# Kernel tuning notes

Hardware: AMD Instinct MI355X
Metric: run time of the kernel (lower is better)

The kernel has to match this reference:

```python
import jax, jax.numpy as jnp
import numpy as np

ORDER = 2
TEMP = 1.0
NEG = -9e15


def setup_inputs() -> dict:
    key = jax.random.key(0)
    ks = jax.random.split(key, 12)
    B, D, N, L = 8, 64, 1024, 12
    C_OUT, NH, S = 64, 2, 2
    NOUT = (NH + 1) * ORDER * S + 1  # 13
    sc = 0.05
    x = jax.random.normal(ks[0], (B, D, N, L), jnp.float32)
    A = jax.random.uniform(ks[1], (S, N, N), jnp.float32)
    support = jnp.where(A > 0.9, A, 0.0)
    nv1 = jax.random.normal(ks[2], (N, D), jnp.float32)
    nv2 = jax.random.normal(ks[3], (D, N), jnp.float32)
    key_w = jax.random.normal(ks[4], (NH, 2 * C_OUT, D, L), jnp.float32) * sc
    key_b = jax.random.normal(ks[5], (NH, 2 * C_OUT), jnp.float32) * sc
    query_w = jax.random.normal(ks[6], (NH, 2 * C_OUT, D, L), jnp.float32) * sc
    query_b = jax.random.normal(ks[7], (NH, 2 * C_OUT), jnp.float32) * sc
    attn_w = jax.random.normal(ks[8], (NOUT, D * NOUT), jnp.float32) * sc
    attn_b = jax.random.normal(ks[9], (NOUT,), jnp.float32) * sc
    final_w = jax.random.normal(ks[10], (C_OUT, D), jnp.float32) * sc
    final_b = jax.random.normal(ks[11], (C_OUT,), jnp.float32) * sc
    return {"x": x, "support": support, "nv1": nv1, "nv2": nv2,
            "key_w": key_w, "key_b": key_b, "query_w": query_w, "query_b": query_b,
            "attn_w": attn_w, "attn_b": attn_b, "final_w": final_w, "final_b": final_b}


def reference(x, support, nv1, nv2, key_w, key_b, query_w, query_b,
              attn_w, attn_b, final_w, final_b):
    B, D, N, L = x.shape
    n_head = key_w.shape[0]
    # spatial PE broadcast: nv1 [N,D] -> [1,D,N,1], nv2 [D,N] -> [1,D,N,1]
    nv1_b = nv1.T[None, :, :, None]
    nv2_b = nv2[None, :, :, None]
    out = [x]
    for s in range(support.shape[0]):
        a = support[s]  # [N,N]
        for ih in range(n_head + 1):
            if ih == 0:
                x1 = x
                for _ in range(ORDER):
                    # x2[b,d,w,l] = sum_v x1[b,d,v,l] * a[v,w]
                    x1 = jnp.einsum('bdvl,vw->bdwl', x1, a)
                    out.append(x1)
            else:
                ki = x + nv1_b
                qi = x + nv2_b
                # Conv2d(c_in, 2*c_out, (1,L)) -> [B, 2*c_out, N]
                keys = jnp.einsum('bdnl,edl->ben', ki, key_w[ih - 1]) + key_b[ih - 1][None, :, None]
                query = jnp.einsum('bdnl,edl->ben', qi, query_w[ih - 1]) + query_b[ih - 1][None, :, None]
                e = jax.nn.relu(jnp.einsum('ben,bem->bnm', keys, query))  # [B,N,N]
                att = jnp.where(a[None] > 0, e, NEG) / TEMP
                att = jax.nn.softmax(att, axis=1)  # normalize over source nodes v
                x1 = x
                for _ in range(ORDER):
                    x1 = jnp.einsum('bdvl,bvw->bdwl', x1, att)
                    out.append(x1)
    H = len(out)  # nout
    # per-branch gating attention (is_attention=True)
    feats = jnp.stack([o.mean(axis=(2, 3)) for o in out], axis=1)  # [B,H,D]
    logits = feats.reshape(B, H * D) @ attn_w.T + attn_b  # [B,H]
    gate = jax.nn.softmax(logits / TEMP, axis=1)
    # SUM head aggregation of gated branches
    h = out[0] * gate[:, 0, None, None, None]
    for i in range(1, H):
        h = h + out[i] * gate[:, i, None, None, None]
    # final 1x1 conv
    h = jnp.einsum('bdnl,od->bonl', h, final_w) + final_b[None, :, None, None]
    return h
```

## Files before the change

### kernel.cpp

```cpp
#include <hip/hip_runtime.h>
#include <hip/hip_bf16.h>

#define BB 8
#define DD 64
#define NNODE 1024
#define LLL 12
#define EE 128
#define NEGV -9.0e15f

typedef _Float16 f16;
typedef _Float16 f16x4 __attribute__((ext_vector_type(4)));
typedef _Float16 f16x8 __attribute__((ext_vector_type(8)));
typedef float f32x4 __attribute__((ext_vector_type(4)));


__device__ __forceinline__ void stage_tile(const char* g, int ld, char* lds, int t) {
    int wid = t >> 6, lane = t & 63;
#pragma unroll
    for (int it = 0; it < 4; it++) {
        int cbase = it * 256 + wid * 64;
        int c = cbase + lane;
        int row = c >> 3, p = c & 7;
        int gch = p ^ (row & 7);
        const char* src = g + (size_t)row * ld + gch * 16;
        char* dst = lds + (size_t)cbase * 16;
        __builtin_amdgcn_global_load_lds(
            (const __attribute__((address_space(1))) unsigned int*)src,
            (__attribute__((address_space(3))) unsigned int*)dst, 16, 0, 0);
    }
}

__device__ __forceinline__ void mma_tile(const char* As, const char* Bs, int t,
                                         f32x4 acc[4][4]) {
    int lane = t & 63, wid = t >> 6;
    int wr = (wid >> 1) * 64, wc = (wid & 1) * 64;
    int lrow = lane & 15, lk = lane >> 4;
#pragma unroll
    for (int kk = 0; kk < 2; kk++) {
        f16x8 af[4], bf[4];
#pragma unroll
        for (int m = 0; m < 4; m++) {
            int row = wr + m * 16 + lrow;
            int p = (kk * 4 + lk) ^ (row & 7);
            af[m] = *(const f16x8*)(As + row * 128 + p * 16);
        }
#pragma unroll
        for (int n = 0; n < 4; n++) {
            int row = wc + n * 16 + lrow;
            int p = (kk * 4 + lk) ^ (row & 7);
            bf[n] = *(const f16x8*)(Bs + row * 128 + p * 16);
        }
#pragma unroll
        for (int m = 0; m < 4; m++)
#pragma unroll
            for (int n = 0; n < 4; n++)
                acc[m][n] = __builtin_amdgcn_mfma_f32_16x16x32_f16(
                    af[m], bf[n], acc[m][n], 0, 0, 0);
    }
}

__device__ __forceinline__ void zero_acc(f32x4 acc[4][4]) {
#pragma unroll
    for (int m = 0; m < 4; m++)
#pragma unroll
        for (int n = 0; n < 4; n++)
#pragma unroll
            for (int q = 0; q < 4; q++) acc[m][n][q] = 0.f;
}

__device__ __forceinline__ const f16* pair_B(const f16* aT, const f16* attT,
                                             int j, int b) {
    if (j == 0) return aT;
    if (j == 3) return aT + 1048576;
    int idx = (j < 3) ? (j - 1) : (j - 2);
    return attT + (size_t)idx * 8388608 + (size_t)b * 1048576;
}


__global__ void k_xt(const float* __restrict__ x, f16* __restrict__ XT,
                     float* __restrict__ xl) {
    int i = blockIdx.x * 256 + threadIdx.x;
    int v = i & 1023, d = (i >> 10) & 63, b = i >> 16;
    const float4* p = reinterpret_cast<const float4*>(x + (size_t)i * 12);
    float4 a = p[0], c = p[1], e = p[2];
    float vv[12] = {a.x, a.y, a.z, a.w, c.x, c.y, c.z, c.w, e.x, e.y, e.z, e.w};
    float ssum = 0.f;
    size_t base = ((size_t)b * 768) * 1024 + v;
    int r0 = d * 12;
#pragma unroll
    for (int l = 0; l < 12; l++) {
        ssum += vv[l];
        XT[base + (size_t)(r0 + l) * 1024] = (f16)vv[l];
    }
    xl[i] = ssum;
}

__global__ __launch_bounds__(256) void k_xt2(const float* __restrict__ x,
                                             f16* __restrict__ xT2) {
    __shared__ f16 Ls[64][208];
    int b = blockIdx.z, d0 = blockIdx.y * 16, n0 = blockIdx.x * 64, t = threadIdx.x;
    for (int f = t; f < 3072; f += 256) {
        int dd = f / 192, rem = f - dd * 192, j = rem / 3, q = rem - j * 3;
        float4 v = *reinterpret_cast<const float4*>(
            x + (((size_t)(b * 64 + d0 + dd) * 1024) + n0 + j) * 12 + q * 4);
        f16* dst = &Ls[j][dd * 12 + q * 4];
        dst[0] = (f16)v.x; dst[1] = (f16)v.y; dst[2] = (f16)v.z; dst[3] = (f16)v.w;
    }
    __syncthreads();
    for (int c = t; c < 1536; c += 256) {
        int j = c / 24, p = c - j * 24;
        *reinterpret_cast<f16x8*>(
            xT2 + ((size_t)(b * 1024) + n0 + j) * 768 + d0 * 12 + p * 8) =
            *reinterpret_cast<const f16x8*>(&Ls[j][p * 8]);
    }
}

__global__ void k_wcvt(const float* __restrict__ kw, const float* __restrict__ qw,
                       float* __restrict__ kwl, f16* __restrict__ kwb) {
    int i = blockIdx.x * 256 + threadIdx.x;
    int d = i & 63, e = (i >> 6) & 127, var = i >> 13;
    const float* src = (var < 2 ? kw + (size_t)var * 98304
                                : qw + (size_t)(var - 2) * 98304) +
                       ((size_t)e * 64 + d) * 12;
    f16* dst = kwb + ((size_t)var * 128 + e) * 768 + d * 12;
    float ssum = 0.f;
#pragma unroll
    for (int l = 0; l < 12; l++) {
        float v = src[l];
        ssum += v;
        dst[l] = (f16)v;
    }
    kwl[i] = ssum;
}

__global__ void k_tkq(const float* __restrict__ kwl, const float* __restrict__ nv1,
                      const float* __restrict__ nv2, const float* __restrict__ kb,
                      const float* __restrict__ qb, float* __restrict__ tkq) {
    int i = blockIdx.x * 256 + threadIdx.x;
    int e = i & 127, n = (i >> 7) & 1023, var = i >> 17;
    float ssum = (var < 2) ? kb[var * 128 + e] : qb[(var - 2) * 128 + e];
    const float* wl = kwl + ((size_t)var * 128 + e) * 64;
    if (var < 2) {
        const float* nvp = nv1 + (size_t)n * 64;
#pragma unroll 8
        for (int d = 0; d < 64; d++) ssum += wl[d] * nvp[d];
    } else {
#pragma unroll 8
        for (int d = 0; d < 64; d++) ssum += wl[d] * nv2[(size_t)d * 1024 + n];
    }
    tkq[i] = ssum;
}

__global__ void k_acvt(const float* __restrict__ sup, f16* __restrict__ aT) {
    __shared__ float Ls[64][65];
    int s = blockIdx.z, v0 = blockIdx.y * 64, w0 = blockIdx.x * 64, t = threadIdx.x;
    int j = t & 63, i0 = t >> 6;
    for (int i = i0; i < 64; i += 4)
        Ls[i][j] = sup[((size_t)s * 1024 + v0 + i) * 1024 + w0 + j];
    __syncthreads();
    for (int i = i0; i < 64; i += 4)
        aT[((size_t)s * 1024 + w0 + i) * 1024 + v0 + j] = (f16)Ls[j][i];
}


__global__ __launch_bounds__(256) void k_kqgemm(const f16* __restrict__ xT2,
                                                const f16* __restrict__ kwb,
                                                const float* __restrict__ tkq,
                                                f16* __restrict__ keysT) {
    __shared__ char As[16384], Bs[16384];
    int z = blockIdx.z, var = z >> 3, b = z & 7;
    int nt = blockIdx.x, t = threadIdx.x;
    const char* Ag = (const char*)(xT2 + ((size_t)b * 1024 + nt * 128) * 768);
    const char* Bg = (const char*)(kwb + (size_t)var * 128 * 768);
    f32x4 acc[4][4];
    zero_acc(acc);
    for (int kt = 0; kt < 12; kt++) {
        stage_tile(Ag + kt * 128, 1536, As, t);
        stage_tile(Bg + kt * 128, 1536, Bs, t);
        __syncthreads();
        mma_tile(As, Bs, t, acc);
        __syncthreads();
    }
    int lane = t & 63, wid = t >> 6;
    int wr = (wid >> 1) * 64, wc = (wid & 1) * 64;
    int cn = lane & 15, rq = (lane >> 4) * 4;
#pragma unroll
    for (int m = 0; m < 4; m++)
#pragma unroll
        for (int q = 0; q < 4; q++) {
            int n_g = nt * 128 + wr + m * 16 + rq + q;
#pragma unroll
            for (int nn = 0; nn < 4; nn++) {
                int e = wc + nn * 16 + cn;
                float v = acc[m][nn][q] + tkq[((size_t)var * 1024 + n_g) * 128 + e];
                keysT[(((size_t)var * 8 + b) * 1024 + n_g) * 128 + e] = (f16)v;
            }
        }
}

__global__ __launch_bounds__(256) void k_scoregemm2(const f16* __restrict__ keysT,
                                                    float* __restrict__ scTall) {
    __shared__ char As[16384], Bs[16384];
    int z = blockIdx.z, h = z >> 3, b = z & 7;
    int wt = blockIdx.y, vt = blockIdx.x, t = threadIdx.x;
    const char* Ag = (const char*)(keysT + (((size_t)(2 + h) * 8 + b) * 1024 + wt * 128) * 128);
    const char* Bg = (const char*)(keysT + (((size_t)h * 8 + b) * 1024 + vt * 128) * 128);
    f32x4 acc[4][4];
    zero_acc(acc);
    for (int kt = 0; kt < 2; kt++) {
        stage_tile(Ag + kt * 128, 256, As, t);
        stage_tile(Bg + kt * 128, 256, Bs, t);
        __syncthreads();
        mma_tile(As, Bs, t, acc);
        __syncthreads();
    }
    int lane = t & 63, wid = t >> 6;
    int wr = (wid >> 1) * 64, wc = (wid & 1) * 64;
    int cn = lane & 15, rq = (lane >> 4) * 4;
#pragma unroll
    for (int m = 0; m < 4; m++)
#pragma unroll
        for (int q = 0; q < 4; q++) {
            int w = wt * 128 + wr + m * 16 + rq + q;
#pragma unroll
            for (int nn = 0; nn < 4; nn++) {
                int v = vt * 128 + wc + nn * 16 + cn;
                scTall[((size_t)z * 1024 + w) * 1024 + v] = fmaxf(acc[m][nn][q], 0.f);
            }
        }
}

__global__ __launch_bounds__(256) void k_prop1m(const f16* __restrict__ ZT,
                                                const f16* __restrict__ aT,
                                                const f16* __restrict__ attT,
                                                f16* __restrict__ P1all) {
    __shared__ char As[16384], Bs[16384];
    int bid = blockIdx.x;
    int swz = (bid & 7) * 288 + (bid >> 3);
    int wt = swz & 7, rt = (swz >> 3) % 6, z = swz / 48;
    int j = z >> 3, b = z & 7;
    int t = threadIdx.x;
    const char* Ag = (const char*)(ZT + ((size_t)b * 768 + rt * 128) * 1024);
    const char* Bg = (const char*)(pair_B(aT, attT, j, b) + (size_t)wt * 128 * 1024);
    f32x4 acc[4][4];
    zero_acc(acc);
    for (int kt = 0; kt < 16; kt++) {
        stage_tile(Ag + kt * 128, 2048, As, t);
        stage_tile(Bg + kt * 128, 2048, Bs, t);
        __syncthreads();
        mma_tile(As, Bs, t, acc);
        __syncthreads();
    }
    f16* P1 = P1all + (size_t)j * 6291456;
    int lane = t & 63, wid = t >> 6;
    int wr = (wid >> 1) * 64, wc = (wid & 1) * 64;
    int cn = lane & 15, rq = (lane >> 4) * 4;
#pragma unroll
    for (int m = 0; m < 4; m++)
#pragma unroll
        for (int q = 0; q < 4; q++) {
            int r = rt * 128 + wr + m * 16 + rq + q;
            size_t pbase = ((size_t)b * 768 + r) * 1024;
#pragma unroll
            for (int nn = 0; nn < 4; nn++) {
                int w = wt * 128 + wc + nn * 16 + cn;
                P1[pbase + w] = (f16)acc[m][nn][q];
            }
        }
}

__global__ __launch_bounds__(256) void k_prop2m(const f16* __restrict__ P1all,
                                                const f16* __restrict__ aT,
                                                const f16* __restrict__ attT,
                                                f16* __restrict__ P2all) {
    __shared__ char As[16384], Bs[16384];
    int bid = blockIdx.x;
    int swz = (bid & 7) * 288 + (bid >> 3);
    int wt = swz & 7, rt = (swz >> 3) % 6, z = swz / 48;
    int j = z >> 3, b = z & 7;
    int t = threadIdx.x;
    const char* Ag = (const char*)(P1all + (size_t)j * 6291456 +
                                   ((size_t)b * 768 + rt * 128) * 1024);
    const char* Bg = (const char*)(pair_B(aT, attT, j, b) + (size_t)wt * 128 * 1024);
    f32x4 acc[4][4];
    zero_acc(acc);
    for (int kt = 0; kt < 16; kt++) {
        stage_tile(Ag + kt * 128, 2048, As, t);
        stage_tile(Bg + kt * 128, 2048, Bs, t);
        __syncthreads();
        mma_tile(As, Bs, t, acc);
        __syncthreads();
    }
    f16* P2 = P2all + (size_t)j * 6291456;
    int lane = t & 63, wid = t >> 6;
    int wr = (wid >> 1) * 64, wc = (wid & 1) * 64;
    int cn = lane & 15, rq = (lane >> 4) * 4;
#pragma unroll
    for (int m = 0; m < 4; m++)
#pragma unroll
        for (int q = 0; q < 4; q++) {
            int r = rt * 128 + wr + m * 16 + rq + q;
            size_t pbase = ((size_t)b * 768 + r) * 1024;
#pragma unroll
            for (int nn = 0; nn < 4; nn++) {
                int w = wt * 128 + wc + nn * 16 + cn;
                P2[pbase + w] = (f16)acc[m][nn][q];
            }
        }
}

__global__ __launch_bounds__(256) void k_prop1g(const f16* __restrict__ A0,
                                                const f16* __restrict__ B0, size_t bsB,
                                                f16* __restrict__ P1) {
    __shared__ char As[16384], Bs[16384];
    int b = blockIdx.z, rt = blockIdx.y, wt = blockIdx.x, t = threadIdx.x;
    const char* Ag = (const char*)(A0 + ((size_t)b * 768 + rt * 128) * 1024);
    const char* Bg = (const char*)(B0 + (size_t)b * bsB + (size_t)wt * 128 * 1024);
    f32x4 acc[4][4];
    zero_acc(acc);
    for (int kt = 0; kt < 16; kt++) {
        stage_tile(Ag + kt * 128, 2048, As, t);
        stage_tile(Bg + kt * 128, 2048, Bs, t);
        __syncthreads();
        mma_tile(As, Bs, t, acc);
        __syncthreads();
    }
    int lane = t & 63, wid = t >> 6;
    int wr = (wid >> 1) * 64, wc = (wid & 1) * 64;
    int cn = lane & 15, rq = (lane >> 4) * 4;
#pragma unroll
    for (int m = 0; m < 4; m++)
#pragma unroll
        for (int q = 0; q < 4; q++) {
            int r = rt * 128 + wr + m * 16 + rq + q;
            size_t pbase = ((size_t)b * 768 + r) * 1024;
#pragma unroll
            for (int nn = 0; nn < 4; nn++) {
                int w = wt * 128 + wc + nn * 16 + cn;
                P1[pbase + w] = (f16)acc[m][nn][q];
            }
        }
}

__global__ __launch_bounds__(256) void k_prop2g(const f16* __restrict__ P1,
                                                const f16* __restrict__ B0, size_t bsB,
                                                f16* __restrict__ hacc,
                                                const float* __restrict__ gate, int gidx) {
    __shared__ char As[16384], Bs[16384];
    int b = blockIdx.z, rt = blockIdx.y, wt = blockIdx.x, t = threadIdx.x;
    const char* Ag = (const char*)(P1 + ((size_t)b * 768 + rt * 128) * 1024);
    const char* Bg = (const char*)(B0 + (size_t)b * bsB + (size_t)wt * 128 * 1024);
    f32x4 acc[4][4];
    zero_acc(acc);
    for (int kt = 0; kt < 16; kt++) {
        stage_tile(Ag + kt * 128, 2048, As, t);
        stage_tile(Bg + kt * 128, 2048, Bs, t);
        __syncthreads();
        mma_tile(As, Bs, t, acc);
        __syncthreads();
    }
    float g1 = gate[b * 13 + gidx], g2 = gate[b * 13 + gidx + 1];
    int lane = t & 63, wid = t >> 6;
    int wr = (wid >> 1) * 64, wc = (wid & 1) * 64;
    int cn = lane & 15, rq = (lane >> 4) * 4;
#pragma unroll
    for (int m = 0; m < 4; m++)
#pragma unroll
        for (int q = 0; q < 4; q++) {
            int r = rt * 128 + wr + m * 16 + rq + q;
            size_t pbase = ((size_t)b * 768 + r) * 1024;
#pragma unroll
            for (int nn = 0; nn < 4; nn++) {
                int w = wt * 128 + wc + nn * 16 + cn;
                float p1v = (float)P1[pbase + w];
                float hv = (float)hacc[pbase + w];
                hacc[pbase + w] = (f16)(hv + g1 * p1v + g2 * acc[m][nn][q]);
            }
        }
}


__global__ void k_softmax3(const float* __restrict__ scTall, const f16* __restrict__ aT,
                           f16* __restrict__ attT) {
    int gw = blockIdx.x * 4 + (threadIdx.x >> 6);
    int w = gw & 1023, hb = gw >> 10;
    int h = hb >> 3, b = hb & 7;
    int lane = threadIdx.x & 63;
    const float* sp = scTall + (size_t)gw * 1024;
    float e[16];
#pragma unroll
    for (int k = 0; k < 16; k++) e[k] = sp[k * 64 + lane];
#pragma unroll
    for (int s = 0; s < 2; s++) {
        const f16* ap = aT + ((size_t)s * 1024 + w) * 1024;
        float xx[16];
        float m = NEGV;
#pragma unroll
        for (int k = 0; k < 16; k++) {
            int v = k * 64 + lane;
            xx[k] = ((float)ap[v] > 0.f) ? e[k] : NEGV;
            m = fmaxf(m, xx[k]);
        }
#pragma unroll
        for (int off = 1; off < 64; off <<= 1) m = fmaxf(m, __shfl_xor(m, off));
        float ssum = 0.f;
#pragma unroll
        for (int k = 0; k < 16; k++) {
            xx[k] = __expf(xx[k] - m);
            ssum += xx[k];
        }
#pragma unroll
        for (int off = 1; off < 64; off <<= 1) ssum += __shfl_xor(ssum, off);
        float inv = 1.f / ssum;
        f16* op = attT + (size_t)(s * 2 + h) * 8388608 +
                  ((size_t)b * 1024 + w) * 1024;
#pragma unroll
        for (int k = 0; k < 16; k++) op[k * 64 + lane] = (f16)(xx[k] * inv);
    }
}

template <int ORDER>
__global__ __launch_bounds__(256) void k_colsum1(
    const f16* __restrict__ aT, const f16* __restrict__ attT,
    const float* __restrict__ ra, const float* __restrict__ ratt,
    float* __restrict__ partial) {
    int u = blockIdx.y, rc = blockIdx.x;
    int t = threadIdx.x;
    int lane7 = t & 127, rh = t >> 7;
    int v0 = lane7 * 8;
    const f16* M = (u < 2) ? aT + (size_t)u * 1048576
                           : attT + (size_t)(u - 2) * 1048576;
    const float* rin = nullptr;
    if (ORDER) rin = (u < 2) ? ra + (size_t)u * 2048 : ratt + (size_t)(u - 2) * 2048;
    float acc[8] = {};
    int row0 = rc * 64 + rh * 32;
#pragma unroll 4
    for (int i = 0; i < 32; i++) {
        int row = row0 + i;
        f16x8 mv = *reinterpret_cast<const f16x8*>(M + (size_t)row * 1024 + v0);
        float sc = ORDER ? rin[row] : 1.f;
#pragma unroll
        for (int j = 0; j < 8; j++) acc[j] += (float)mv[j] * sc;
    }
    float* pp = partial + ((size_t)u * 32 + rc * 2 + rh) * 1024 + v0;
#pragma unroll
    for (int j = 0; j < 8; j++) pp[j] = acc[j];
}

template <int ORDER>
__global__ void k_colsum2(const float* __restrict__ partial, float* __restrict__ ra,
                          float* __restrict__ ratt) {
    int u = blockIdx.x, t = threadIdx.x;
    for (int v = t; v < 1024; v += 256) {
        float s = 0.f;
#pragma unroll
        for (int k = 0; k < 32; k++) s += partial[((size_t)u * 32 + k) * 1024 + v];
        float* out = (u < 2) ? ra + (size_t)u * 2048 : ratt + (size_t)(u - 2) * 2048;
        out[ORDER * 1024 + v] = s;
    }
}

__global__ void k_feat13(const float* __restrict__ xl, const float* __restrict__ ra,
                         const float* __restrict__ ratt, float* __restrict__ feats) {
    int bd = blockIdx.x;
    int b = bd >> 6, d = bd & 63;
    const float* xp = xl + (size_t)bd * 1024;
    int t = threadIdx.x;
    float s[13];
#pragma unroll
    for (int i = 0; i < 13; i++) s[i] = 0.f;
    for (int v = t; v < 1024; v += 256) {
        float xv = xp[v];
        s[0] += xv;
#pragma unroll
        for (int ss = 0; ss < 2; ss++) {
            s[1 + ss * 6 + 0] += xv * ra[ss * 2048 + v];
            s[1 + ss * 6 + 1] += xv * ra[ss * 2048 + 1024 + v];
#pragma unroll
            for (int hh = 0; hh < 2; hh++) {
                const float* rb = ratt + (((size_t)(ss * 2 + hh) * 8 + b)) * 2048;
                s[1 + ss * 6 + 2 + hh * 2] += xv * rb[v];
                s[1 + ss * 6 + 3 + hh * 2] += xv * rb[1024 + v];
            }
        }
    }
    int wid = t >> 6, lane = t & 63;
#pragma unroll
    for (int i = 0; i < 13; i++)
#pragma unroll
        for (int off = 1; off < 64; off <<= 1) s[i] += __shfl_xor(s[i], off);
    __shared__ float red[13][4];
    if (lane == 0)
#pragma unroll
        for (int i = 0; i < 13; i++) red[i][wid] = s[i];
    __syncthreads();
    if (t < 13) {
        float tot = red[t][0] + red[t][1] + red[t][2] + red[t][3];
        feats[(size_t)b * 832 + t * 64 + d] = tot * (1.f / (1024.f * 12.f));
    }
}

__global__ void k_gate(const float* __restrict__ feats, const float* __restrict__ aw,
                       const float* __restrict__ ab, float* __restrict__ gate) {
    int b = blockIdx.x, t = threadIdx.x;
    __shared__ float lg[13];
    if (t < 13) {
        float s = ab[t];
        const float* f = feats + (size_t)b * 832;
        const float* w = aw + (size_t)t * 832;
        for (int k = 0; k < 832; k++) s += f[k] * w[k];
        lg[t] = s;
    }
    __syncthreads();
    if (t == 0) {
        float m = lg[0];
        for (int j = 1; j < 13; j++) m = fmaxf(m, lg[j]);
        float ss = 0.f;
        for (int j = 0; j < 13; j++) ss += __expf(lg[j] - m);
        float inv = 1.f / ss;
        for (int j = 0; j < 13; j++) gate[b * 13 + j] = __expf(lg[j] - m) * inv;
    }
}

__global__ __launch_bounds__(256) void k_zt2(f16* __restrict__ XT,
                                             const float* __restrict__ fw) {
    __shared__ f16 xs[64][136];
    __shared__ float fws[64][64];
    int nt = blockIdx.x, l = blockIdx.y, b = blockIdx.z;
    int t = threadIdx.x;
    f16* base = XT + (size_t)b * 786432 + (size_t)l * 1024 + nt * 128;
#pragma unroll
    for (int it = 0; it < 4; it++) {
        int idx = it * 256 + t;
        int row = idx >> 4, c = idx & 15;
        *reinterpret_cast<f16x8*>(&xs[row][c * 8]) =
            *reinterpret_cast<const f16x8*>(base + (size_t)row * 12288 + c * 8);
    }
    for (int i = t; i < 4096; i += 256) ((float*)fws)[i] = fw[i];
    __syncthreads();
    int nl = t & 31, og = t >> 5;
    float acc[8][4];
#pragma unroll
    for (int oo = 0; oo < 8; oo++)
#pragma unroll
        for (int j = 0; j < 4; j++) acc[oo][j] = 0.f;
#pragma unroll 4
    for (int d = 0; d < 64; d++) {
        f16x4 xv = *reinterpret_cast<const f16x4*>(&xs[d][nl * 4]);
        float x0 = (float)xv[0], x1 = (float)xv[1], x2 = (float)xv[2], x3 = (float)xv[3];
#pragma unroll
        for (int oo = 0; oo < 8; oo++) {
            float w = fws[og * 8 + oo][d];
            acc[oo][0] += w * x0; acc[oo][1] += w * x1;
            acc[oo][2] += w * x2; acc[oo][3] += w * x3;
        }
    }
#pragma unroll
    for (int oo = 0; oo < 8; oo++) {
        int o = og * 8 + oo;
        f16x4 ov;
        ov[0] = (f16)acc[oo][0]; ov[1] = (f16)acc[oo][1];
        ov[2] = (f16)acc[oo][2]; ov[3] = (f16)acc[oo][3];
        *reinterpret_cast<f16x4*>(base + (size_t)o * 12288 + nl * 4) = ov;
    }
}

__global__ void k_out(const f16* __restrict__ ZT, const f16* __restrict__ P1all,
                      const f16* __restrict__ P2all, const float* __restrict__ gate,
                      const float* __restrict__ fb, float* __restrict__ out) {
    int idx = blockIdx.x * 256 + threadIdx.x;
    int n = idx & 1023, o = (idx >> 10) & 63, b = idx >> 16;
    const float* g = gate + b * 13;
    size_t rowbase = ((size_t)b * 768 + o * 12) * 1024 + n;
    float v[12];
    float g0 = g[0], fbv = fb[o];
#pragma unroll
    for (int l = 0; l < 12; l++)
        v[l] = fbv + g0 * (float)ZT[rowbase + (size_t)l * 1024];
#pragma unroll
    for (int j = 0; j < 6; j++) {
        float g1 = g[1 + 2 * j], g2 = g[2 + 2 * j];
        const f16* p1 = P1all + (size_t)j * 6291456 + rowbase;
        const f16* p2 = P2all + (size_t)j * 6291456 + rowbase;
#pragma unroll
        for (int l = 0; l < 12; l++)
            v[l] += g1 * (float)p1[(size_t)l * 1024] + g2 * (float)p2[(size_t)l * 1024];
    }
    float4* dst = reinterpret_cast<float4*>(out + (((size_t)b * 64 + o) * 1024 + n) * 12);
    float4 o0 = {v[0], v[1], v[2], v[3]};
    float4 o1 = {v[4], v[5], v[6], v[7]};
    float4 o2 = {v[8], v[9], v[10], v[11]};
    dst[0] = o0; dst[1] = o1; dst[2] = o2;
}

__global__ void k_hinit2(const f16* __restrict__ ZT, const float* __restrict__ gate,
                         f16* __restrict__ hacc) {
    size_t i8 = (size_t)blockIdx.x * 256 + threadIdx.x;
    int b = (int)(i8 / 98304);
    float g = gate[b * 13];
    f16x8 v = *reinterpret_cast<const f16x8*>(ZT + i8 * 8);
    f16x8 o;
#pragma unroll
    for (int j = 0; j < 8; j++) o[j] = (f16)(g * (float)v[j]);
    *reinterpret_cast<f16x8*>(hacc + i8 * 8) = o;
}

__global__ void k_biasout(const f16* __restrict__ hacc, const float* __restrict__ fb,
                          float* __restrict__ out) {
    int idx = blockIdx.x * 256 + threadIdx.x;
    int n = idx & 1023, o = (idx >> 10) & 63, b = idx >> 16;
    float fbv = fb[o];
    float v[12];
#pragma unroll
    for (int l = 0; l < 12; l++)
        v[l] = (float)hacc[((size_t)b * 768 + o * 12 + l) * 1024 + n] + fbv;
    float4* dst = reinterpret_cast<float4*>(out + (((size_t)b * 64 + o) * 1024 + n) * 12);
    float4 o0 = {v[0], v[1], v[2], v[3]};
    float4 o1 = {v[4], v[5], v[6], v[7]};
    float4 o2 = {v[8], v[9], v[10], v[11]};
    dst[0] = o0; dst[1] = o1; dst[2] = o2;
}


extern "C" void kernel_launch(void* const* d_in, const int* in_sizes, int n_in,
                              void* d_out, int out_size, void* d_ws, size_t ws_size,
                              hipStream_t stream) {
    const float* x   = (const float*)d_in[0];
    const float* sup = (const float*)d_in[1];
    const float* nv1 = (const float*)d_in[2];
    const float* nv2 = (const float*)d_in[3];
    const float* kw  = (const float*)d_in[4];
    const float* kb  = (const float*)d_in[5];
    const float* qw  = (const float*)d_in[6];
    const float* qb  = (const float*)d_in[7];
    const float* aw  = (const float*)d_in[8];
    const float* ab  = (const float*)d_in[9];
    const float* fw  = (const float*)d_in[10];
    const float* fb  = (const float*)d_in[11];
    float* hout = (float*)d_out;

    float* wsf = (float*)d_ws;
    size_t o = 0;
    f16*   XT     = (f16*)(wsf + o);  o += 3145728;
    float* attReg = wsf + o;          o += 16777216;
    f16*   attT   = (f16*)attReg;
    f16*   xT2    = (f16*)attReg;
    f16*   aT     = (f16*)(wsf + o);  o += 1048576;
    float* gate   = wsf + o;          o += 128;
    size_t rc = o;
    size_t oA = rc;
    float* scTall = wsf + oA;          oA += 16777216;
    f16*   keysT  = (f16*)(wsf + oA);  oA += 2097152;
    f16*   kwb    = (f16*)(wsf + oA);  oA += 196608;
    float* kwl    = wsf + oA;          oA += 32768;
    float* tkq    = wsf + oA;          oA += 524288;
    float* xl     = wsf + oA;          oA += 524288;
    float* ra     = wsf + oA;          oA += 4096;
    float* ratt   = wsf + oA;          oA += 65536;
    float* feats  = wsf + oA;          oA += 6656;
    float* partial= wsf + oA;          oA += 1114112;
    size_t oBm = rc;
    f16*   P1all  = (f16*)(wsf + oBm); oBm += 18874368;
    f16*   P2all  = (f16*)(wsf + oBm); oBm += 18874368;
    size_t oBf = rc;
    f16*   P1f    = (f16*)(wsf + oBf); oBf += 3145728;
    f16*   haccf  = (f16*)(wsf + oBf); oBf += 3145728;
    size_t needMega = (oA > oBm ? oA : oBm) * 4;
    size_t needFall = (oA > oBf ? oA : oBf) * 4;
    bool mega = ws_size >= needMega;
    if (!mega && ws_size < needFall) return;

    f16* ZT = XT;

    k_xt<<<2048, 256, 0, stream>>>(x, XT, xl);
    k_xt2<<<dim3(16, 4, 8), 256, 0, stream>>>(x, xT2);
    k_wcvt<<<128, 256, 0, stream>>>(kw, qw, kwl, kwb);
    k_tkq<<<2048, 256, 0, stream>>>(kwl, nv1, nv2, kb, qb, tkq);
    k_acvt<<<dim3(16, 16, 2), 256, 0, stream>>>(sup, aT);

    k_kqgemm<<<dim3(8, 1, 32), 256, 0, stream>>>(xT2, kwb, tkq, keysT);

    k_scoregemm2<<<dim3(8, 8, 16), 256, 0, stream>>>(keysT, scTall);
    k_softmax3<<<4096, 256, 0, stream>>>(scTall, aT, attT);

    k_colsum1<0><<<dim3(16, 34), 256, 0, stream>>>(aT, attT, ra, ratt, partial);
    k_colsum2<0><<<34, 256, 0, stream>>>(partial, ra, ratt);
    k_colsum1<1><<<dim3(16, 34), 256, 0, stream>>>(aT, attT, ra, ratt, partial);
    k_colsum2<1><<<34, 256, 0, stream>>>(partial, ra, ratt);
    k_feat13<<<512, 256, 0, stream>>>(xl, ra, ratt, feats);
    k_gate<<<8, 64, 0, stream>>>(feats, aw, ab, gate);

    k_zt2<<<dim3(8, 12, 8), 256, 0, stream>>>(XT, fw);

    if (mega) {
        k_prop1m<<<2304, 256, 0, stream>>>(ZT, aT, attT, P1all);
        k_prop2m<<<2304, 256, 0, stream>>>(P1all, aT, attT, P2all);
        k_out<<<2048, 256, 0, stream>>>(ZT, P1all, P2all, gate, fb, hout);
    } else {
        k_hinit2<<<3072, 256, 0, stream>>>(ZT, gate, haccf);
        for (int s = 0; s < 2; s++)
            for (int kind = 0; kind < 3; kind++) {
                const f16* B0;
                size_t bsB;
                if (kind == 0) { B0 = aT + (size_t)s * 1048576; bsB = 0; }
                else { B0 = attT + (size_t)((s * 2 + kind - 1) * 8) * 1048576; bsB = 1048576; }
                int g1 = 1 + s * 6 + 2 * kind;
                k_prop1g<<<dim3(8, 6, 8), 256, 0, stream>>>(ZT, B0, bsB, P1f);
                k_prop2g<<<dim3(8, 6, 8), 256, 0, stream>>>(P1f, B0, bsB, haccf, gate, g1);
            }
        k_biasout<<<2048, 256, 0, stream>>>(haccf, fb, hout);
    }
}
```

Baseline: 381.0 us.

## Add 256x256-tile pipelined propagation GEMM and fold gating into second pass

New measurement: 392.4 us. 1.03x slower.

```diff
diff --git a/kernel.cpp b/kernel.cpp
--- a/kernel.cpp
+++ b/kernel.cpp
@@ -74,6 +74,142 @@
     if (j == 3) return aT + 1048576;
     int idx = (j < 3) ? (j - 1) : (j - 2);
     return attT + (size_t)idx * 8388608 + (size_t)b * 1048576;
+}
+
+
+__device__ __forceinline__ void stage_half(const char* g, char* dlds, int t) {
+    int wid = t >> 6, lane = t & 63;
+#pragma unroll
+    for (int it = 0; it < 2; it++) {
+        int cbase = it * 512 + wid * 64;
+        int c = cbase + lane;
+        int row = c >> 3, p = c & 7;
+        int gch = p ^ (row & 7);
+        const char* src = g + (size_t)row * 2048 + gch * 16;
+        char* dst = dlds + (size_t)cbase * 16;
+        __builtin_amdgcn_global_load_lds(
+            (const __attribute__((address_space(1))) unsigned int*)src,
+            (__attribute__((address_space(3))) unsigned int*)dst, 16, 0, 0);
+    }
+}
+
+#define BARR do { asm volatile("" ::: "memory"); __builtin_amdgcn_s_barrier(); \
+                  asm volatile("" ::: "memory"); } while (0)
+#define VM4  asm volatile("s_waitcnt vmcnt(4)" ::: "memory")
+
+#define MF1(M2,N2,KK,QM,QN,BS) \
+    acc[(QM)*4+(M2)][(QN)*2+(N2)] = __builtin_amdgcn_mfma_f32_16x16x32_f16( \
+        a[M2][KK], BS[N2][KK], acc[(QM)*4+(M2)][(QN)*2+(N2)], 0, 0, 0);
+#define MFQ(QM,QN,BS) \
+  MF1(0,0,0,QM,QN,BS) MF1(0,0,1,QM,QN,BS) MF1(0,1,0,QM,QN,BS) MF1(0,1,1,QM,QN,BS) \
+  MF1(1,0,0,QM,QN,BS) MF1(1,0,1,QM,QN,BS) MF1(1,1,0,QM,QN,BS) MF1(1,1,1,QM,QN,BS) \
+  MF1(2,0,0,QM,QN,BS) MF1(2,0,1,QM,QN,BS) MF1(2,1,0,QM,QN,BS) MF1(2,1,1,QM,QN,BS) \
+  MF1(3,0,0,QM,QN,BS) MF1(3,0,1,QM,QN,BS) MF1(3,1,0,QM,QN,BS) MF1(3,1,1,QM,QN,BS)
+
+#define DSA1(M,KK,SET,BUF) { int row_ = ((SET)*4+(M))*16 + lrow; \
+    int p_ = ((KK)*4+lk) ^ (row_ & 7); \
+    a[M][KK] = *(const f16x8*)(lds + (BUF)*65536 + gm*16384 + row_*128 + p_*16); }
+#define DSA(SET,BUF) DSA1(0,0,SET,BUF) DSA1(0,1,SET,BUF) DSA1(1,0,SET,BUF) \
+    DSA1(1,1,SET,BUF) DSA1(2,0,SET,BUF) DSA1(2,1,SET,BUF) DSA1(3,0,SET,BUF) DSA1(3,1,SET,BUF)
+
+#define DSB1(BS,N2,KK,PAIR,BUF) { int row_ = (gn&1)*64 + ((PAIR)*2+(N2))*16 + lrow; \
+    int p_ = ((KK)*4+lk) ^ (row_ & 7); \
+    BS[N2][KK] = *(const f16x8*)(lds + (BUF)*65536 + 32768 + (gn>>1)*16384 + row_*128 + p_*16); }
+#define DSB(BS,PAIR,BUF) DSB1(BS,0,0,PAIR,BUF) DSB1(BS,0,1,PAIR,BUF) \
+    DSB1(BS,1,0,PAIR,BUF) DSB1(BS,1,1,PAIR,BUF)
+
+#define STG(BUF,ISB,HALF,KT) { \
+    const char* g_ = ((ISB) ? Bgc : Agc) + (size_t)((HALF)*128)*2048 + (KT)*128; \
+    char* d_ = lds + (BUF)*65536 + (ISB)*32768 + (HALF)*16384; \
+    stage_half(g_, d_, t); }
+
+template <int MODE>
+__global__ __launch_bounds__(512, 2) void k_prop8(
+        const f16* __restrict__ Asrc, const f16* __restrict__ aT,
+        const f16* __restrict__ attT, f16* __restrict__ out,
+        const f16* __restrict__ P1rd, const float* __restrict__ gate) {
+    extern __shared__ char lds[];
+    int bid = blockIdx.x;
+    int swz = (bid & 7) * 72 + (bid >> 3);
+    int z = swz / 12, rem = swz - z * 12;
+    int rt = rem >> 2, wt = rem & 3;
+    int j = z >> 3, b = z & 7;
+    int t = threadIdx.x;
+    int lane = t & 63, wid = t >> 6;
+    int lrow = lane & 15, lk = lane >> 4;
+    int gm = wid >> 2, gn = wid & 3;
+
+    const f16* Abase = MODE
+        ? (Asrc + (((size_t)j * 8 + b) * 768 + rt * 256) * 1024)
+        : (Asrc + ((size_t)b * 768 + rt * 256) * 1024);
+    const char* Agc = (const char*)Abase;
+    const char* Bgc = (const char*)(pair_B(aT, attT, j, b) + (size_t)wt * 256 * 1024);
+
+    f32x4 acc[8][4];
+#pragma unroll
+    for (int m = 0; m < 8; m++)
+#pragma unroll
+        for (int n = 0; n < 4; n++)
+#pragma unroll
+            for (int q = 0; q < 4; q++) acc[m][n][q] = 0.f;
+
+    STG(0, 0, 0, 0) STG(0, 0, 1, 0) STG(0, 1, 0, 0) STG(0, 1, 1, 0)
+    STG(1, 1, 0, 1) STG(1, 1, 1, 1)
+
+    f16x8 a[4][2], b01[2][2], b23[2][2];
+
+    for (int it = 0; it < 8; it++) {
+        int kt1 = 2 * it + 1;
+        int kt2 = (2 * it + 2) & 15;
+        int kt3 = (2 * it + 3) & 15;
+        VM4; BARR;
+        DSA(0, 0) DSB(b01, 0, 0)
+        STG(1, 0, 0, kt1)
+        BARR; __builtin_amdgcn_s_setprio(1); MFQ(0, 0, b01) __builtin_amdgcn_s_setprio(0); BARR;
+        DSB(b23, 1, 0)
+        STG(1, 0, 1, kt1)
+        BARR; __builtin_amdgcn_s_setprio(1); MFQ(0, 1, b23) __builtin_amdgcn_s_setprio(0); BARR;
+        DSA(1, 0)
+        STG(0, 1, 0, kt2)
+        BARR; __builtin_amdgcn_s_setprio(1); MFQ(1, 0, b01) __builtin_amdgcn_s_setprio(0); BARR;
+        STG(0, 1, 1, kt2)
+        BARR; __builtin_amdgcn_s_setprio(1); MFQ(1, 1, b23) __builtin_amdgcn_s_setprio(0); BARR;
+        VM4; BARR;
+        DSA(0, 1) DSB(b01, 0, 1)
+        STG(0, 0, 0, kt2)
+        BARR; __builtin_amdgcn_s_setprio(1); MFQ(0, 0, b01) __builtin_amdgcn_s_setprio(0); BARR;
+        DSB(b23, 1, 1)
+        STG(0, 0, 1, kt2)
+        BARR; __builtin_amdgcn_s_setprio(1); MFQ(0, 1, b23) __builtin_amdgcn_s_setprio(0); BARR;
+        DSA(1, 1)
+        STG(1, 1, 0, kt3)
+        BARR; __builtin_amdgcn_s_setprio(1); MFQ(1, 0, b01) __builtin_amdgcn_s_setprio(0); BARR;
+        STG(1, 1, 1, kt3)
+        BARR; __builtin_amdgcn_s_setprio(1); MFQ(1, 1, b23) __builtin_amdgcn_s_setprio(0); BARR;
+    }
+
+    float g1 = 0.f, g2 = 0.f;
+    if (MODE) {
+        int gidx = 1 + (j >= 3 ? 6 : 0) + 2 * (j % 3);
+        g1 = gate[b * 13 + gidx];
+        g2 = gate[b * 13 + gidx + 1];
+    }
+    size_t obase = (size_t)j * 6291456;
+#pragma unroll
+    for (int m = 0; m < 8; m++)
+#pragma unroll
+        for (int q = 0; q < 4; q++) {
+            int r = rt * 256 + gm * 128 + m * 16 + lk * 4 + q;
+            size_t pbase = obase + ((size_t)b * 768 + r) * 1024;
+#pragma unroll
+            for (int n = 0; n < 4; n++) {
+                int w = wt * 256 + gn * 64 + n * 16 + lrow;
+                if (MODE)
+                    out[pbase + w] = (f16)(g1 * (float)P1rd[pbase + w] + g2 * acc[m][n][q]);
+                else
+                    out[pbase + w] = (f16)acc[m][n][q];
+            }
+        }
 }
 
 
@@ -272,7 +408,8 @@
 __global__ __launch_bounds__(256) void k_prop2m(const f16* __restrict__ P1all,
                                                 const f16* __restrict__ aT,
                                                 const f16* __restrict__ attT,
-                                                f16* __restrict__ P2all) {
+                                                f16* __restrict__ Hpart,
+                                                const float* __restrict__ gate) {
     __shared__ char As[16384], Bs[16384];
     int bid = blockIdx.x;
     int swz = (bid & 7) * 288 + (bid >> 3);
@@ -291,7 +428,10 @@
         mma_tile(As, Bs, t, acc);
         __syncthreads();
     }
-    f16* P2 = P2all + (size_t)j * 6291456;
+    int gidx = 1 + (j >= 3 ? 6 : 0) + 2 * (j % 3);
+    float g1 = gate[b * 13 + gidx], g2 = gate[b * 13 + gidx + 1];
+    const f16* P1 = P1all + (size_t)j * 6291456;
+    f16* Hp = Hpart + (size_t)j * 6291456;
     int lane = t & 63, wid = t >> 6;
     int wr = (wid >> 1) * 64, wc = (wid & 1) * 64;
     int cn = lane & 15, rq = (lane >> 4) * 4;
@@ -304,77 +444,7 @@
 #pragma unroll
             for (int nn = 0; nn < 4; nn++) {
                 int w = wt * 128 + wc + nn * 16 + cn;
-                P2[pbase + w] = (f16)acc[m][nn][q];
-            }
-        }
-}
-
-__global__ __launch_bounds__(256) void k_prop1g(const f16* __restrict__ A0,
-                                                const f16* __restrict__ B0, size_t bsB,
-                                                f16* __restrict__ P1) {
-    __shared__ char As[16384], Bs[16384];
-    int b = blockIdx.z, rt = blockIdx.y, wt = blockIdx.x, t = threadIdx.x;
-    const char* Ag = (const char*)(A0 + ((size_t)b * 768 + rt * 128) * 1024);
-    const char* Bg = (const char*)(B0 + (size_t)b * bsB + (size_t)wt * 128 * 1024);
-    f32x4 acc[4][4];
-    zero_acc(acc);
-    for (int kt = 0; kt < 16; kt++) {
-        stage_tile(Ag + kt * 128, 2048, As, t);
-        stage_tile(Bg + kt * 128, 2048, Bs, t);
-        __syncthreads();
-        mma_tile(As, Bs, t, acc);
-        __syncthreads();
-    }
-    int lane = t & 63, wid = t >> 6;
-    int wr = (wid >> 1) * 64, wc = (wid & 1) * 64;
-    int cn = lane & 15, rq = (lane >> 4) * 4;
-#pragma unroll
-    for (int m = 0; m < 4; m++)
-#pragma unroll
-        for (int q = 0; q < 4; q++) {
-            int r = rt * 128 + wr + m * 16 + rq + q;
-            size_t pbase = ((size_t)b * 768 + r) * 1024;
-#pragma unroll
-            for (int nn = 0; nn < 4; nn++) {
-                int w = wt * 128 + wc + nn * 16 + cn;
-                P1[pbase + w] = (f16)acc[m][nn][q];
-            }
-        }
-}
-
-__global__ __launch_bounds__(256) void k_prop2g(const f16* __restrict__ P1,
-                                                const f16* __restrict__ B0, size_t bsB,
-                                                f16* __restrict__ hacc,
-                                                const float* __restrict__ gate, int gidx) {
-    __shared__ char As[16384], Bs[16384];
-    int b = blockIdx.z, rt = blockIdx.y, wt = blockIdx.x, t = threadIdx.x;
-    const char* Ag = (const char*)(P1 + ((size_t)b * 768 + rt * 128) * 1024);
-    const char* Bg = (const char*)(B0 + (size_t)b * bsB + (size_t)wt * 128 * 1024);
-    f32x4 acc[4][4];
-    zero_acc(acc);
-    for (int kt = 0; kt < 16; kt++) {
-        stage_tile(Ag + kt * 128, 2048, As, t);
-        stage_tile(Bg + kt * 128, 2048, Bs, t);
-        __syncthreads();
-        mma_tile(As, Bs, t, acc);
-        __syncthreads();
-    }
-    float g1 = gate[b * 13 + gidx], g2 = gate[b * 13 + gidx + 1];
-    int lane = t & 63, wid = t >> 6;
-    int wr = (wid >> 1) * 64, wc = (wid & 1) * 64;
-    int cn = lane & 15, rq = (lane >> 4) * 4;
-#pragma unroll
-    for (int m = 0; m < 4; m++)
-#pragma unroll
-        for (int q = 0; q < 4; q++) {
-            int r = rt * 128 + wr + m * 16 + rq + q;
-            size_t pbase = ((size_t)b * 768 + r) * 1024;
-#pragma unroll
-            for (int nn = 0; nn < 4; nn++) {
-                int w = wt * 128 + wc + nn * 16 + cn;
-                float p1v = (float)P1[pbase + w];
-                float hv = (float)hacc[pbase + w];
-                hacc[pbase + w] = (f16)(hv + g1 * p1v + g2 * acc[m][nn][q]);
+                Hp[pbase + w] = (f16)(g1 * (float)P1[pbase + w] + g2 * acc[m][nn][q]);
             }
         }
 }
@@ -565,55 +635,23 @@
     }
 }
 
-__global__ void k_out(const f16* __restrict__ ZT, const f16* __restrict__ P1all,
-                      const f16* __restrict__ P2all, const float* __restrict__ gate,
-                      const float* __restrict__ fb, float* __restrict__ out) {
+__global__ void k_out2(const f16* __restrict__ ZT, const f16* __restrict__ Hp,
+                       const float* __restrict__ gate, const float* __restrict__ fb,
+                       float* __restrict__ out) {
     int idx = blockIdx.x * 256 + threadIdx.x;
     int n = idx & 1023, o = (idx >> 10) & 63, b = idx >> 16;
-    const float* g = gate + b * 13;
+    float g0 = gate[b * 13], fbv = fb[o];
     size_t rowbase = ((size_t)b * 768 + o * 12) * 1024 + n;
     float v[12];
-    float g0 = g[0], fbv = fb[o];
 #pragma unroll
     for (int l = 0; l < 12; l++)
         v[l] = fbv + g0 * (float)ZT[rowbase + (size_t)l * 1024];
 #pragma unroll
     for (int j = 0; j < 6; j++) {
-        float g1 = g[1 + 2 * j], g2 = g[2 + 2 * j];
-        const f16* p1 = P1all + (size_t)j * 6291456 + rowbase;
-        const f16* p2 = P2all + (size_t)j * 6291456 + rowbase;
-#pragma unroll
-        for (int l = 0; l < 12; l++)
-            v[l] += g1 * (float)p1[(size_t)l * 1024] + g2 * (float)p2[(size_t)l * 1024];
-    }
-    float4* dst = reinterpret_cast<float4*>(out + (((size_t)b * 64 + o) * 1024 + n) * 12);
-    float4 o0 = {v[0], v[1], v[2], v[3]};
-    float4 o1 = {v[4], v[5], v[6], v[7]};
-    float4 o2 = {v[8], v[9], v[10], v[11]};
-    dst[0] = o0; dst[1] = o1; dst[2] = o2;
-}
-
-__global__ void k_hinit2(const f16* __restrict__ ZT, const float* __restrict__ gate,
-                         f16* __restrict__ hacc) {
-    size_t i8 = (size_t)blockIdx.x * 256 + threadIdx.x;
-    int b = (int)(i8 / 98304);
-    float g = gate[b * 13];
-    f16x8 v = *reinterpret_cast<const f16x8*>(ZT + i8 * 8);
-    f16x8 o;
-#pragma unroll
-    for (int j = 0; j < 8; j++) o[j] = (f16)(g * (float)v[j]);
-    *reinterpret_cast<f16x8*>(hacc + i8 * 8) = o;
-}
-
-__global__ void k_biasout(const f16* __restrict__ hacc, const float* __restrict__ fb,
-                          float* __restrict__ out) {
-    int idx = blockIdx.x * 256 + threadIdx.x;
-    int n = idx & 1023, o = (idx >> 10) & 63, b = idx >> 16;
-    float fbv = fb[o];
-    float v[12];
-#pragma unroll
-    for (int l = 0; l < 12; l++)
-        v[l] = (float)hacc[((size_t)b * 768 + o * 12 + l) * 1024 + n] + fbv;
+        const f16* p = Hp + (size_t)j * 6291456 + rowbase;
+#pragma unroll
+        for (int l = 0; l < 12; l++) v[l] += (float)p[(size_t)l * 1024];
+    }
     float4* dst = reinterpret_cast<float4*>(out + (((size_t)b * 64 + o) * 1024 + n) * 12);
     float4 o0 = {v[0], v[1], v[2], v[3]};
     float4 o1 = {v[4], v[5], v[6], v[7]};
@@ -659,16 +697,17 @@
     float* ratt   = wsf + oA;          oA += 65536;
     float* feats  = wsf + oA;          oA += 6656;
     float* partial= wsf + oA;          oA += 1114112;
-    size_t oBm = rc;
-    f16*   P1all  = (f16*)(wsf + oBm); oBm += 18874368;
-    f16*   P2all  = (f16*)(wsf + oBm); oBm += 18874368;
-    size_t oBf = rc;
-    f16*   P1f    = (f16*)(wsf + oBf); oBf += 3145728;
-    f16*   haccf  = (f16*)(wsf + oBf); oBf += 3145728;
-    size_t needMega = (oA > oBm ? oA : oBm) * 4;
-    size_t needFall = (oA > oBf ? oA : oBf) * 4;
-    bool mega = ws_size >= needMega;
-    if (!mega && ws_size < needFall) return;
+    size_t oB = rc;
+    f16*   P1all  = (f16*)(wsf + oB); oB += 18874368;
+    f16*   Hpart  = (f16*)(wsf + oB); oB += 18874368;
+    size_t need = ((oA > oB) ? oA : oB) * 4;
+    if (ws_size < need) return;
+
+    bool use8 =
+        (hipFuncSetAttribute(reinterpret_cast<const void*>(k_prop8<0>),
+                             hipFuncAttributeMaxDynamicSharedMemorySize, 131072) == hipSuccess) &&
+        (hipFuncSetAttribute(reinterpret_cast<const void*>(k_prop8<1>),
+                             hipFuncAttributeMaxDynamicSharedMemorySize, 131072) == hipSuccess);
 
     f16* ZT = XT;
 
@@ -692,22 +731,12 @@
 
     k_zt2<<<dim3(8, 12, 8), 256, 0, stream>>>(XT, fw);
 
-    if (mega) {
+    if (use8) {
+        k_prop8<0><<<576, 512, 131072, stream>>>(ZT, aT, attT, P1all, (const f16*)nullptr, gate);
+        k_prop8<1><<<576, 512, 131072, stream>>>(P1all, aT, attT, Hpart, P1all, gate);
+    } else {
         k_prop1m<<<2304, 256, 0, stream>>>(ZT, aT, attT, P1all);
-        k_prop2m<<<2304, 256, 0, stream>>>(P1all, aT, attT, P2all);
-        k_out<<<2048, 256, 0, stream>>>(ZT, P1all, P2all, gate, fb, hout);
-    } else {
-        k_hinit2<<<3072, 256, 0, stream>>>(ZT, gate, haccf);
-        for (int s = 0; s < 2; s++)
-            for (int kind = 0; kind < 3; kind++) {
-                const f16* B0;
-                size_t bsB;
-                if (kind == 0) { B0 = aT + (size_t)s * 1048576; bsB = 0; }
-                else { B0 = attT + (size_t)((s * 2 + kind - 1) * 8) * 1048576; bsB = 1048576; }
-                int g1 = 1 + s * 6 + 2 * kind;
-                k_prop1g<<<dim3(8, 6, 8), 256, 0, stream>>>(ZT, B0, bsB, P1f);
-                k_prop2g<<<dim3(8, 6, 8), 256, 0, stream>>>(P1f, B0, bsB, haccf, gate, g1);
-            }
-        k_biasout<<<2048, 256, 0, stream>>>(haccf, fb, hout);
-    }
-}
+        k_prop2m<<<2304, 256, 0, stream>>>(P1all, aT, attT, Hpart, gate);
+    }
+    k_out2<<<2048, 256, 0, stream>>>(ZT, Hpart, gate, fb, hout);
+}
```
